# Optimization experiments

Measured on AMD Instinct MI355X. Metric: run time of the kernel, lower is better.

## Reference

```python
import jax, jax.numpy as jnp
import numpy as np

NUM_MAIN_SEQ_ATOMS = 12   # backbone atoms per RNA residue
NUM_NEIGHBOUR = 30
EMBEDDING_DIM = 32
EPS = 1e-5
BIG_DIST = 1000000.0


def setup_inputs() -> dict:
    key = jax.random.key(0)
    k1, k2, k3 = jax.random.split(key, 3)
    B, L, A = 2, 256, NUM_MAIN_SEQ_ATOMS
    coords = jax.random.normal(k1, (B, L, A, 3), dtype=jnp.float32) * 10.0
    mask = jax.random.randint(k2, (B, L), 0, 2).astype(jnp.int32)
    emb_table = jax.random.normal(k3, (NUM_MAIN_SEQ_ATOMS, EMBEDDING_DIM), dtype=jnp.float32)
    scale = jnp.ones((1, 1, EMBEDDING_DIM), dtype=jnp.float32)
    shift = jnp.zeros((1, 1, EMBEDDING_DIM), dtype=jnp.float32)
    return {"coords": coords, "mask": mask, "emb_table": emb_table,
            "scale": scale, "shift": shift}


def _graph_norm(features, m, scale, shift):
    # features: (B,N,E); m: (B,N) float {0,1}
    mm = m[:, :, None]                                   # (B,N,1)
    masked = features * mm
    cnt = jnp.maximum(mm.sum(axis=1, keepdims=True), 1.0)  # (B,1,1)
    mean = masked.sum(axis=1, keepdims=True) / cnt
    var = ((masked - mean) ** 2).sum(axis=1, keepdims=True) / cnt
    std = jnp.sqrt(var + EPS)
    out = ((features - mean) / std) * scale + shift
    return out * mm


def reference(coords, mask, emb_table, scale, shift):
    B, L, A, _ = coords.shape
    N = L * A
    atom_coords = coords.reshape(B, N, 3)
    atom_mask = jnp.repeat(mask, A, axis=1)              # (B,N) int
    m = atom_mask.astype(coords.dtype)

    # ---- encoder: cyclic atom-type embedding + graph norm ----
    atom_types = jnp.arange(N) % A                       # (N,)
    emb = emb_table[atom_types][None] * m[:, :, None]    # (B,N,E)
    encode = _graph_norm(emb, m, scale, shift)

    # ---- kNN graph: O(N^2) pairwise distances + masked top-k ----
    d = atom_coords[:, None, :, :] - atom_coords[:, :, None, :]  # (B,N,N,3)
    dist = jnp.sqrt((d ** 2).sum(-1) + 1e-6)             # (B,N,N)
    m2 = m[:, None, :] * m[:, :, None]                   # (B,N,N)
    dist = dist * m2 + (1.0 - m2) * BIG_DIST

    k = min(NUM_NEIGHBOUR, N)
    neg_d, edge_idx = jax.lax.top_k(-dist, k)            # smallest-k
    dist_neighbors = -neg_d                              # (B,N,k)

    pad = (atom_mask == 0)[:, :, None]                   # (B,N,1)
    edge_idx = jnp.where(pad, 0, edge_idx)
    dist_neighbors = jnp.where(pad, BIG_DIST, dist_neighbors)
    return atom_coords, atom_mask, encode, dist_neighbors, edge_idx
```

## Files before the change

kernel.cpp:

```cpp
#include <hip/hip_runtime.h>
#include <math.h>

#define NA   12
#define NL   256
#define NN   3072
#define NB   2
#define ED   32
#define KNB  30
#define BIGD 1000000.0f

#define OFF_COORDS 0
#define OFF_MASK   18432
#define OFF_ENC    24576
#define OFF_DIST   221184
#define OFF_IDX    405504

#define KEYVAL 0xFFFFF000u
#define KEYIDX 0x00000FFFu
#define MASKED_D2 1e12f

static __device__ __forceinline__ unsigned umin32(unsigned a, unsigned b) {
    return a < b ? a : b;
}

#define DPP_MIN_STEP(CTRL)                                                        \
    {                                                                             \
        int t_ = __builtin_amdgcn_update_dpp(v_, v_, (CTRL), 0xf, 0xf, false);    \
        v_ = (int)umin32((unsigned)v_, (unsigned)t_);                             \
    }

#define TREE8(A0,A1,A2,A3,A4,A5,A6,A7) \
    umin32(umin32(umin32((A0),(A1)), umin32((A2),(A3))), \
           umin32(umin32((A4),(A5)), umin32((A6),(A7))))

#define REMOVE_RESCAN(G)                                                          \
    {                                                                             \
        _Pragma("unroll")                                                         \
        for (int u = 0; u < 8; ++u) {                                             \
            const int t = (G) * 8 + u;                                            \
            k[t] = (k[t] == wkey) ? 0xFFFFFFFFu : k[t];                           \
        }                                                                         \
        gm[(G)] = TREE8(k[(G)*8+0],k[(G)*8+1],k[(G)*8+2],k[(G)*8+3],              \
                        k[(G)*8+4],k[(G)*8+5],k[(G)*8+6],k[(G)*8+7]);             \
    }

__global__ __launch_bounds__(512, 4) void fused_kernel(const float* __restrict__ coords,
                                                       const int* __restrict__ mask,
                                                       const float* __restrict__ emb,
                                                       const float* __restrict__ scale,
                                                       const float* __restrict__ shift,
                                                       float* __restrict__ out) {
    __shared__ float4 sc4[NN];

    int tid  = threadIdx.x;
    int lane = tid & 63;
    int wave = tid >> 6;
    int b    = (int)(blockIdx.x) / 384;
    int rblk = (int)(blockIdx.x) - b * 384;
    const float* cb = coords + (size_t)b * NN * 3;
    const int*   mb = mask + b * NL;

#pragma unroll
    for (int s = 0; s < 6; ++s) {
        int e = tid + s * 512;
        int r = (e * 43691) >> 19;
        float4 p;
        p.x = cb[e * 3 + 0];
        p.y = cb[e * 3 + 1];
        p.z = cb[e * 3 + 2];
        p.w = (float)mb[r];
        sc4[e] = p;
    }
    __syncthreads();

    int i   = rblk * 8 + wave;
    int row = b * NN + i;
    float4 q = sc4[i];

    if (q.w != 0.f) {
        unsigned k[48];
        unsigned gm[6];

#pragma unroll
        for (int t = 0; t < 48; ++t) {
            int j = t * 64 + lane;
            float4 v = sc4[j];
            float dx = v.x - q.x, dy = v.y - q.y, dz = v.z - q.z;
            float s = dx * dx + dy * dy + dz * dz + 1e-6f;
            s = (v.w != 0.f) ? s : MASKED_D2;
            k[t] = (__float_as_uint(s) & KEYVAL) | (unsigned)j;
        }
#pragma unroll
        for (int g = 0; g < 6; ++g)
            gm[g] = TREE8(k[g*8+0],k[g*8+1],k[g*8+2],k[g*8+3],
                          k[g*8+4],k[g*8+5],k[g*8+6],k[g*8+7]);

        unsigned cur = umin32(umin32(umin32(gm[0], gm[1]), umin32(gm[2], gm[3])),
                              umin32(gm[4], gm[5]));
        unsigned rkey = 0u;

        for (int it = 0; it < KNB; ++it) {
            int v_ = (int)cur;
            DPP_MIN_STEP(0xB1)
            DPP_MIN_STEP(0x4E)
            DPP_MIN_STEP(0x141)
            DPP_MIN_STEP(0x140)
            unsigned r0  = (unsigned)__builtin_amdgcn_readlane(v_, 0);
            unsigned r16 = (unsigned)__builtin_amdgcn_readlane(v_, 16);
            unsigned r32 = (unsigned)__builtin_amdgcn_readlane(v_, 32);
            unsigned r48 = (unsigned)__builtin_amdgcn_readlane(v_, 48);
            unsigned wkey = umin32(umin32(r0, r16), umin32(r32, r48));
            rkey = (lane == it) ? wkey : rkey;

            int wg = (int)((wkey & KEYIDX) >> 9);
            switch (wg) {
                case 0: REMOVE_RESCAN(0); break;
                case 1: REMOVE_RESCAN(1); break;
                case 2: REMOVE_RESCAN(2); break;
                case 3: REMOVE_RESCAN(3); break;
                case 4: REMOVE_RESCAN(4); break;
                default: REMOVE_RESCAN(5); break;
            }
            cur = umin32(umin32(umin32(gm[0], gm[1]), umin32(gm[2], gm[3])),
                         umin32(gm[4], gm[5]));
        }

        if (lane < KNB) {
            float d2 = __uint_as_float(rkey & KEYVAL);
            out[OFF_DIST + (size_t)row * KNB + lane] = sqrtf(d2);
            out[OFF_IDX  + (size_t)row * KNB + lane] = (float)(rkey & KEYIDX);
        }
    } else {
        if (lane < KNB) {
            out[OFF_DIST + (size_t)row * KNB + lane] = BIGD;
            out[OFF_IDX  + (size_t)row * KNB + lane] = 0.f;
        }
    }

    int gidx = (int)blockIdx.x * 512 + tid;

    if (gidx < NB * NN * ED) {
        int bb = (gidx >> 5) >= NN ? 1 : 0;
        const int4* m4 = (const int4*)(mask + bb * NL);
        int4 mv = m4[lane];
        float S = (float)(mv.x + mv.y + mv.z + mv.w);
#pragma unroll
        for (int m = 1; m < 64; m <<= 1) S += __shfl_xor(S, m);

        int c = gidx & (ED - 1);
        float e[NA];
        float colsum = 0.f;
#pragma unroll
        for (int a = 0; a < NA; ++a) { e[a] = emb[a * ED + c]; colsum += e[a]; }
        float cnt  = fmaxf(12.0f * S, 1.0f);
        float mean = S * colsum / cnt;
        float acc  = 0.f;
#pragma unroll
        for (int a = 0; a < NA; ++a) { float dd = e[a] - mean; acc += dd * dd; }
        float var  = (S * acc + ((float)NN - 12.0f * S) * mean * mean) / cnt;
        float rstd = 1.0f / sqrtf(var + 1e-5f);

        int n  = (gidx >> 5) - bb * NN;
        int nr = (n * 43691) >> 19;
        int mi = mask[bb * NL + nr];
        float v = 0.f;
        if (mi) {
            float en = emb[(n - nr * NA) * ED + c];
            v = (en - mean) * rstd * scale[c] + shift[c];
        }
        out[OFF_ENC + gidx] = v;
    }

    if (gidx < NB * NN * 3) {
        out[OFF_COORDS + gidx] = coords[gidx];
    }

    if (gidx < NB * NN) {
        int bb = gidx >= NN ? 1 : 0;
        int nn = gidx - bb * NN;
        int nr = (nn * 43691) >> 19;
        out[OFF_MASK + gidx] = (float)mask[bb * NL + nr];
    }
}

extern "C" void kernel_launch(void* const* d_in, const int* in_sizes, int n_in,
                              void* d_out, int out_size, void* d_ws, size_t ws_size,
                              hipStream_t stream) {
    const float* coords = (const float*)d_in[0];
    const int*   mask   = (const int*)d_in[1];
    const float* emb    = (const float*)d_in[2];
    const float* scale  = (const float*)d_in[3];
    const float* shift  = (const float*)d_in[4];
    float* out = (float*)d_out;

    fused_kernel<<<NB * (NN / 8), 512, 0, stream>>>(coords, mask, emb, scale, shift, out);
}
```

Baseline: 87.61 us.

## Process two rows per wave, halve grid, vectorize coord staging into LDS

Each wave now computes the kNN top-k for two query rows serially, so the grid shrinks from 768 to 384 blocks and the per-block LDS staging of the full coordinate set is amortized over twice the rows. Coordinate staging switches to float4 global loads that are repacked into xyz+mask entries. The graph-norm path reads the atom mask from LDS and computes the variance in a single pass using sums and sums of squares. The risk is worse load balance and less latency hiding: 384 blocks do not divide evenly over the CUs, and each wave's top-k work becomes a longer serial chain.

Result: slower. 102.6 us (+17.2%).

```diff
diff --git a/kernel.cpp b/kernel.cpp
--- a/kernel.cpp
+++ b/kernel.cpp
@@ -55,116 +55,121 @@
     int tid  = threadIdx.x;
     int lane = tid & 63;
     int wave = tid >> 6;
-    int b    = (int)(blockIdx.x) / 384;
-    int rblk = (int)(blockIdx.x) - b * 384;
-    const float* cb = coords + (size_t)b * NN * 3;
-    const int*   mb = mask + b * NL;
-
-#pragma unroll
-    for (int s = 0; s < 6; ++s) {
-        int e = tid + s * 512;
-        int r = (e * 43691) >> 19;
-        float4 p;
-        p.x = cb[e * 3 + 0];
-        p.y = cb[e * 3 + 1];
-        p.z = cb[e * 3 + 2];
-        p.w = (float)mb[r];
-        sc4[e] = p;
+    int b    = (int)(blockIdx.x) / 192;
+    int rblk = (int)(blockIdx.x) - b * 192;
+    const float4* cg4 = (const float4*)(coords + (size_t)b * NN * 3);
+    const int*    mb  = mask + b * NL;
+
+    for (int task = tid; task < NN / 4; task += 512) {
+        float4 f0 = cg4[3 * task + 0];
+        float4 f1 = cg4[3 * task + 1];
+        float4 f2 = cg4[3 * task + 2];
+        int base = 4 * task;
+        float m0 = (float)mb[((base + 0) * 43691) >> 19];
+        float m1 = (float)mb[((base + 1) * 43691) >> 19];
+        float m2 = (float)mb[((base + 2) * 43691) >> 19];
+        float m3 = (float)mb[((base + 3) * 43691) >> 19];
+        sc4[base + 0] = make_float4(f0.x, f0.y, f0.z, m0);
+        sc4[base + 1] = make_float4(f0.w, f1.x, f1.y, m1);
+        sc4[base + 2] = make_float4(f1.z, f1.w, f2.x, m2);
+        sc4[base + 3] = make_float4(f2.y, f2.z, f2.w, m3);
     }
     __syncthreads();
 
-    int i   = rblk * 8 + wave;
-    int row = b * NN + i;
-    float4 q = sc4[i];
-
-    if (q.w != 0.f) {
-        unsigned k[48];
-        unsigned gm[6];
-
-#pragma unroll
-        for (int t = 0; t < 48; ++t) {
-            int j = t * 64 + lane;
-            float4 v = sc4[j];
-            float dx = v.x - q.x, dy = v.y - q.y, dz = v.z - q.z;
-            float s = dx * dx + dy * dy + dz * dz + 1e-6f;
-            s = (v.w != 0.f) ? s : MASKED_D2;
-            k[t] = (__float_as_uint(s) & KEYVAL) | (unsigned)j;
+#pragma unroll 1
+    for (int rr = 0; rr < 2; ++rr) {
+        int i   = rblk * 16 + wave + rr * 8;
+        int row = b * NN + i;
+        float4 q = sc4[i];
+
+        if (q.w != 0.f) {
+            unsigned k[48];
+            unsigned gm[6];
+
+#pragma unroll
+            for (int t = 0; t < 48; ++t) {
+                int j = t * 64 + lane;
+                float4 v = sc4[j];
+                float dx = v.x - q.x, dy = v.y - q.y, dz = v.z - q.z;
+                float s = dx * dx + dy * dy + dz * dz + 1e-6f;
+                s = (v.w != 0.f) ? s : MASKED_D2;
+                k[t] = (__float_as_uint(s) & KEYVAL) | (unsigned)j;
+            }
+#pragma unroll
+            for (int g = 0; g < 6; ++g)
+                gm[g] = TREE8(k[g*8+0],k[g*8+1],k[g*8+2],k[g*8+3],
+                              k[g*8+4],k[g*8+5],k[g*8+6],k[g*8+7]);
+
+            unsigned cur = umin32(umin32(umin32(gm[0], gm[1]), umin32(gm[2], gm[3])),
+                                  umin32(gm[4], gm[5]));
+            unsigned rkey = 0u;
+
+            for (int it = 0; it < KNB; ++it) {
+                int v_ = (int)cur;
+                DPP_MIN_STEP(0xB1)
+                DPP_MIN_STEP(0x4E)
+                DPP_MIN_STEP(0x141)
+                DPP_MIN_STEP(0x140)
+                unsigned r0  = (unsigned)__builtin_amdgcn_readlane(v_, 0);
+                unsigned r16 = (unsigned)__builtin_amdgcn_readlane(v_, 16);
+                unsigned r32 = (unsigned)__builtin_amdgcn_readlane(v_, 32);
+                unsigned r48 = (unsigned)__builtin_amdgcn_readlane(v_, 48);
+                unsigned wkey = umin32(umin32(r0, r16), umin32(r32, r48));
+                rkey = (lane == it) ? wkey : rkey;
+
+                int wg = (int)((wkey & KEYIDX) >> 9);
+                switch (wg) {
+                    case 0: REMOVE_RESCAN(0); break;
+                    case 1: REMOVE_RESCAN(1); break;
+                    case 2: REMOVE_RESCAN(2); break;
+                    case 3: REMOVE_RESCAN(3); break;
+                    case 4: REMOVE_RESCAN(4); break;
+                    default: REMOVE_RESCAN(5); break;
+                }
+                cur = umin32(umin32(umin32(gm[0], gm[1]), umin32(gm[2], gm[3])),
+                             umin32(gm[4], gm[5]));
+            }
+
+            if (lane < KNB) {
+                float d2 = __uint_as_float(rkey & KEYVAL);
+                out[OFF_DIST + (size_t)row * KNB + lane] = sqrtf(d2);
+                out[OFF_IDX  + (size_t)row * KNB + lane] = (float)(rkey & KEYIDX);
+            }
+        } else {
+            if (lane < KNB) {
+                out[OFF_DIST + (size_t)row * KNB + lane] = BIGD;
+                out[OFF_IDX  + (size_t)row * KNB + lane] = 0.f;
+            }
         }
-#pragma unroll
-        for (int g = 0; g < 6; ++g)
-            gm[g] = TREE8(k[g*8+0],k[g*8+1],k[g*8+2],k[g*8+3],
-                          k[g*8+4],k[g*8+5],k[g*8+6],k[g*8+7]);
-
-        unsigned cur = umin32(umin32(umin32(gm[0], gm[1]), umin32(gm[2], gm[3])),
-                              umin32(gm[4], gm[5]));
-        unsigned rkey = 0u;
-
-        for (int it = 0; it < KNB; ++it) {
-            int v_ = (int)cur;
-            DPP_MIN_STEP(0xB1)
-            DPP_MIN_STEP(0x4E)
-            DPP_MIN_STEP(0x141)
-            DPP_MIN_STEP(0x140)
-            unsigned r0  = (unsigned)__builtin_amdgcn_readlane(v_, 0);
-            unsigned r16 = (unsigned)__builtin_amdgcn_readlane(v_, 16);
-            unsigned r32 = (unsigned)__builtin_amdgcn_readlane(v_, 32);
-            unsigned r48 = (unsigned)__builtin_amdgcn_readlane(v_, 48);
-            unsigned wkey = umin32(umin32(r0, r16), umin32(r32, r48));
-            rkey = (lane == it) ? wkey : rkey;
-
-            int wg = (int)((wkey & KEYIDX) >> 9);
-            switch (wg) {
-                case 0: REMOVE_RESCAN(0); break;
-                case 1: REMOVE_RESCAN(1); break;
-                case 2: REMOVE_RESCAN(2); break;
-                case 3: REMOVE_RESCAN(3); break;
-                case 4: REMOVE_RESCAN(4); break;
-                default: REMOVE_RESCAN(5); break;
-            }
-            cur = umin32(umin32(umin32(gm[0], gm[1]), umin32(gm[2], gm[3])),
-                         umin32(gm[4], gm[5]));
-        }
-
-        if (lane < KNB) {
-            float d2 = __uint_as_float(rkey & KEYVAL);
-            out[OFF_DIST + (size_t)row * KNB + lane] = sqrtf(d2);
-            out[OFF_IDX  + (size_t)row * KNB + lane] = (float)(rkey & KEYIDX);
-        }
-    } else {
-        if (lane < KNB) {
-            out[OFF_DIST + (size_t)row * KNB + lane] = BIGD;
-            out[OFF_IDX  + (size_t)row * KNB + lane] = 0.f;
-        }
     }
 
     int gidx = (int)blockIdx.x * 512 + tid;
 
-    if (gidx < NB * NN * ED) {
-        int bb = (gidx >> 5) >= NN ? 1 : 0;
-        const int4* m4 = (const int4*)(mask + bb * NL);
+    {
+        const int4* m4 = (const int4*)(mask + b * NL);
         int4 mv = m4[lane];
         float S = (float)(mv.x + mv.y + mv.z + mv.w);
 #pragma unroll
         for (int m = 1; m < 64; m <<= 1) S += __shfl_xor(S, m);
 
         int c = gidx & (ED - 1);
-        float e[NA];
-        float colsum = 0.f;
-#pragma unroll
-        for (int a = 0; a < NA; ++a) { e[a] = emb[a * ED + c]; colsum += e[a]; }
+        float colsum = 0.f, sumsq = 0.f;
+#pragma unroll
+        for (int a = 0; a < NA; ++a) {
+            float e = emb[a * ED + c];
+            colsum += e; sumsq += e * e;
+        }
         float cnt  = fmaxf(12.0f * S, 1.0f);
         float mean = S * colsum / cnt;
-        float acc  = 0.f;
-#pragma unroll
-        for (int a = 0; a < NA; ++a) { float dd = e[a] - mean; acc += dd * dd; }
+        float acc  = sumsq - 2.0f * mean * colsum + 12.0f * mean * mean;
         float var  = (S * acc + ((float)NN - 12.0f * S) * mean * mean) / cnt;
         float rstd = 1.0f / sqrtf(var + 1e-5f);
 
-        int n  = (gidx >> 5) - bb * NN;
+        int n  = (gidx >> 5) - b * NN;
         int nr = (n * 43691) >> 19;
-        int mi = mask[bb * NL + nr];
+        float mi = sc4[n].w;
         float v = 0.f;
-        if (mi) {
+        if (mi != 0.f) {
             float en = emb[(n - nr * NA) * ED + c];
             v = (en - mean) * rstd * scale[c] + shift[c];
         }
@@ -193,5 +198,5 @@
     const float* shift  = (const float*)d_in[4];
     float* out = (float*)d_out;
 
-    fused_kernel<<<NB * (NN / 8), 512, 0, stream>>>(coords, mask, emb, scale, shift, out);
+    fused_kernel<<<NB * (NN / 16), 512, 0, stream>>>(coords, mask, emb, scale, shift, out);
 }
```
